# Performance work log

Measured on AMD Instinct MI355X. Metric: run time of the kernel, lower is better.

## Reference

```python
import jax, jax.numpy as jnp
import numpy as np

D_MODEL = 1024
N_HEADS = 16
D_HEAD = D_MODEL // N_HEADS


def setup_inputs() -> dict:
    key = jax.random.key(0)
    ks = jax.random.split(key, 11)
    B, S = 4, 2048
    scale = 1.0 / np.sqrt(D_MODEL)
    inp = {
        "query": jax.random.normal(ks[0], (B, S, D_MODEL), jnp.float32),
        "key": jax.random.normal(ks[1], (B, S, D_MODEL), jnp.float32),
        "value": jax.random.normal(ks[2], (B, S, D_MODEL), jnp.float32),
        "Wq": jax.random.normal(ks[3], (D_MODEL, D_MODEL), jnp.float32) * scale,
        "bq": jnp.zeros((D_MODEL,), jnp.float32),
        "Wk": jax.random.normal(ks[4], (D_MODEL, D_MODEL), jnp.float32) * scale,
        "bk": jnp.zeros((D_MODEL,), jnp.float32),
        "Wv": jax.random.normal(ks[5], (D_MODEL, D_MODEL), jnp.float32) * scale,
        "bv": jnp.zeros((D_MODEL,), jnp.float32),
        "Wo": jax.random.normal(ks[6], (D_MODEL, D_MODEL), jnp.float32) * scale,
        "bo": jnp.zeros((D_MODEL,), jnp.float32),
    }
    return inp


def _split_heads(x):
    b, s, _ = x.shape
    return x.reshape(b, s, N_HEADS, D_HEAD).transpose(0, 2, 1, 3)  # [b,h,s,dh]


def reference(query, key, value, Wq, bq, Wk, bk, Wv, bv, Wo, bo):
    Q = _split_heads(query @ Wq + bq)
    K = _split_heads(key @ Wk + bk)
    V = _split_heads(value @ Wv + bv)
    scores = jnp.einsum("bhqd,bhkd->bhqk", Q, K) / jnp.sqrt(jnp.float32(D_HEAD))
    attn = jax.nn.softmax(scores, axis=-1)  # dropout p=0 (eval)
    context = jnp.einsum("bhqk,bhkd->bhqd", attn, V)
    b, h, s, dh = context.shape
    context = context.transpose(0, 2, 1, 3).reshape(b, s, D_MODEL)
    return context @ Wo + bo
```

## Files before the change

### kernel.cpp

```cpp
#include <hip/hip_runtime.h>
#include <stdint.h>

#define DM 1024
#define SEQ 2048
#define MTOT 8192

typedef __attribute__((ext_vector_type(8))) short bf16x8;
typedef __attribute__((ext_vector_type(4))) float f32x4;
typedef __attribute__((ext_vector_type(16))) float f32x16;
typedef __attribute__((ext_vector_type(8))) unsigned short u16x8;
typedef __attribute__((ext_vector_type(4))) unsigned short u16x4;
typedef __attribute__((ext_vector_type(4))) uint32_t u32x4;

__device__ __forceinline__ unsigned short f2bf(float x) {
  uint32_t u = __builtin_bit_cast(uint32_t, x);
  u += 0x7fffu + ((u >> 16) & 1u);
  return (unsigned short)(u >> 16);
}

__device__ __forceinline__ uint32_t cvtpk_bf16(float lo, float hi) {
  uint32_t r;
  asm("v_cvt_pk_bf16_f32 %0, %1, %2" : "=v"(r) : "v"(lo), "v"(hi));
  return r;
}

__device__ __forceinline__ void gload16(void* lds, const void* g) {
  __builtin_amdgcn_global_load_lds(
      (const __attribute__((address_space(1))) void*)(uintptr_t)g,
      (__attribute__((address_space(3))) void*)(uintptr_t)lds,
      16, 0, 0);
}

__global__ __launch_bounds__(256)
void prep_w(const float* __restrict__ w0, const float* __restrict__ w1,
            const float* __restrict__ w2, const float* __restrict__ w3,
            unsigned short* __restrict__ Wt) {
  const int z = blockIdx.z;
  const float* W = z == 0 ? w0 : z == 1 ? w1 : z == 2 ? w2 : w3;
  unsigned short* out = Wt + (size_t)z * 1048576;
  __shared__ float tile[32][33];
  const int n0 = blockIdx.x * 32, k0 = blockIdx.y * 32;
  const int tx = threadIdx.x & 31, ty = threadIdx.x >> 5;
#pragma unroll
  for (int j = 0; j < 32; j += 8)
    tile[ty + j][tx] = W[(size_t)(k0 + ty + j) * DM + n0 + tx];
  __syncthreads();
#pragma unroll
  for (int j = 0; j < 32; j += 8)
    out[(size_t)(n0 + ty + j) * DM + k0 + tx] = f2bf(tile[tx][ty + j]);
}

__global__ __launch_bounds__(256)
void cvt_f32_bf16(const float* __restrict__ in, unsigned short* __restrict__ out, int n8) {
  int i = blockIdx.x * 256 + threadIdx.x;
  if (i < n8) {
    f32x4 a = *(const f32x4*)(in + (size_t)i * 8);
    f32x4 b = *(const f32x4*)(in + (size_t)i * 8 + 4);
    u16x8 o;
#pragma unroll
    for (int j = 0; j < 4; ++j) { o[j] = f2bf(a[j]); o[4 + j] = f2bf(b[j]); }
    *(u16x8*)(out + (size_t)i * 8) = o;
  }
}

template <int MODE>
__global__ __launch_bounds__(256)
void gemm_bt(const unsigned short* __restrict__ A,
             const unsigned short* __restrict__ Wt,
             const float* __restrict__ bias,
             void* __restrict__ C, float oscale) {
  __shared__ char sA[16384];
  __shared__ char sB[16384];
  const int t = threadIdx.x, wave = t >> 6, lane = t & 63;
  const int m0 = blockIdx.y * 128, n0 = blockIdx.x * 128;
  const int wr = (wave >> 1) * 64, wc = (wave & 1) * 64;
  const int lr = lane & 15, kg = lane >> 4;

  f32x4 acc[4][4];
#pragma unroll
  for (int i = 0; i < 4; ++i)
#pragma unroll
    for (int j = 0; j < 4; ++j) acc[i][j] = (f32x4){0.f, 0.f, 0.f, 0.f};

  for (int kt = 0; kt < 16; ++kt) {
    __syncthreads();
#pragma unroll
    for (int i = 0; i < 4; ++i) {
      int c = wave * 4 + i;
      int row = c * 8 + (lane >> 3);
      int bo = ((lane & 7) * 16) ^ ((row & 7) << 4);
      gload16(&sA[c * 1024], (const char*)(A + (size_t)(m0 + row) * DM + kt * 64) + bo);
      gload16(&sB[c * 1024], (const char*)(Wt + (size_t)(n0 + row) * DM + kt * 64) + bo);
    }
    __syncthreads();
#pragma unroll
    for (int ks = 0; ks < 2; ++ks) {
      bf16x8 afr[4], bfr[4];
#pragma unroll
      for (int j = 0; j < 4; ++j) {
        int mr = wr + j * 16 + lr;
        afr[j] = *(const bf16x8*)&sA[mr * 128 + ((ks * 64 + kg * 16) ^ ((mr & 7) << 4))];
        int nr = wc + j * 16 + lr;
        bfr[j] = *(const bf16x8*)&sB[nr * 128 + ((ks * 64 + kg * 16) ^ ((nr & 7) << 4))];
      }
#pragma unroll
      for (int mi = 0; mi < 4; ++mi)
#pragma unroll
        for (int nj = 0; nj < 4; ++nj)
          acc[mi][nj] = __builtin_amdgcn_mfma_f32_16x16x32_bf16(afr[mi], bfr[nj], acc[mi][nj], 0, 0, 0);
    }
  }
#pragma unroll
  for (int nj = 0; nj < 4; ++nj) {
    int col = n0 + wc + nj * 16 + lr;
    float bv = bias[col];
#pragma unroll
    for (int mi = 0; mi < 4; ++mi) {
      int rowseq = m0 + wr + mi * 16 + kg * 4;
      if (MODE == 2) {
        u16x4 pk;
#pragma unroll
        for (int r = 0; r < 4; ++r) pk[r] = f2bf(acc[mi][nj][r] + bv);
        *(u16x4*)((unsigned short*)C +
                  ((size_t)((rowseq >> 11) << 10) + col) * SEQ + (rowseq & 2047)) = pk;
      } else {
#pragma unroll
        for (int r = 0; r < 4; ++r) {
          float v = (acc[mi][nj][r] + bv) * oscale;
          if (MODE == 1) ((float*)C)[(size_t)(rowseq + r) * DM + col] = v;
          else ((unsigned short*)C)[(size_t)(rowseq + r) * DM + col] = f2bf(v);
        }
      }
    }
  }
}

__global__ __launch_bounds__(512)
void attn(const unsigned short* __restrict__ Qb,
          const unsigned short* __restrict__ Kb,
          const unsigned short* __restrict__ Vt,
          unsigned short* __restrict__ Ctx) {
  __shared__ char sK[2][8192];
  __shared__ char sV[2][8192];
  const int t = threadIdx.x, wave = t >> 6, lane = t & 63;
  const int l31 = lane & 31, hi = lane >> 5;
  const int bh = blockIdx.x, b = bh >> 4, h = bh & 15;
  const int q0 = blockIdx.y * 256;

  const int srow = wave * 8 + (lane >> 3);
  const int sbo = ((lane & 7) * 16) ^ ((srow & 7) << 4);
  const char* gK = (const char*)(Kb + (size_t)b * SEQ * DM + h * 64) + (size_t)srow * (DM * 2) + sbo;
  const char* gV = (const char*)(Vt + ((size_t)bh * 64 + srow) * SEQ) + sbo;

  bf16x8 qf[4];
  {
    const unsigned short* qp = Qb + ((size_t)b * SEQ + q0 + wave * 32 + l31) * DM + h * 64 + hi * 8;
#pragma unroll
    for (int ks = 0; ks < 4; ++ks) qf[ks] = *(const bf16x8*)(qp + ks * 16);
  }

  f32x16 ot0, ot1;
#pragma unroll
  for (int i = 0; i < 16; ++i) { ot0[i] = 0.f; ot1[i] = 0.f; }
  float m = -1e30f, l = 0.f;

  gload16(&sK[0][wave * 1024], gK);
  gload16(&sV[0][wave * 1024], gV);
  __syncthreads();

  for (int kt = 0; kt < SEQ / 64; ++kt) {
    const int pb = kt & 1;
    if (kt + 1 < SEQ / 64) {
      gload16(&sK[pb ^ 1][wave * 1024], gK + (size_t)(kt + 1) * 64 * (DM * 2));
      gload16(&sV[pb ^ 1][wave * 1024], gV + (size_t)(kt + 1) * 128);
    }

    f32x16 s0, s1;
#pragma unroll
    for (int i = 0; i < 16; ++i) { s0[i] = 0.f; s1[i] = 0.f; }
    const char* kbase = sK[pb];
#pragma unroll
    for (int ks = 0; ks < 4; ++ks) {
      const int swz = (ks * 32 + hi * 16) ^ ((l31 & 7) << 4);
      bf16x8 kf0 = *(const bf16x8*)(kbase + l31 * 128 + swz);
      s0 = __builtin_amdgcn_mfma_f32_32x32x16_bf16(kf0, qf[ks], s0, 0, 0, 0);
      bf16x8 kf1 = *(const bf16x8*)(kbase + (32 + l31) * 128 + swz);
      s1 = __builtin_amdgcn_mfma_f32_32x32x16_bf16(kf1, qf[ks], s1, 0, 0, 0);
    }

    float pmax = s0[0];
#pragma unroll
    for (int i = 1; i < 16; ++i) pmax = fmaxf(pmax, s0[i]);
#pragma unroll
    for (int i = 0; i < 16; ++i) pmax = fmaxf(pmax, s1[i]);
    pmax = fmaxf(pmax, __shfl_xor(pmax, 32));
    if (__any(pmax > m + 8.f)) {
      float mn = fmaxf(m, pmax);
      float al = __builtin_amdgcn_exp2f(m - mn);
      m = mn; l *= al;
#pragma unroll
      for (int i = 0; i < 16; ++i) { ot0[i] *= al; ot1[i] *= al; }
    }
    float sum = 0.f;
#pragma unroll
    for (int i = 0; i < 16; ++i) { float p = __builtin_amdgcn_exp2f(s0[i] - m); s0[i] = p; sum += p; }
#pragma unroll
    for (int i = 0; i < 16; ++i) { float p = __builtin_amdgcn_exp2f(s1[i] - m); s1[i] = p; sum += p; }
    sum += __shfl_xor(sum, 32);
    l += sum;

    const char* vbase = sV[pb];
#pragma unroll
    for (int sl = 0; sl < 4; ++sl) {
      const f32x16& sp = (sl < 2) ? s0 : s1;
      const int s8 = (sl & 1) * 8;
      uint32_t x0 = cvtpk_bf16(sp[s8 + 0], sp[s8 + 1]);
      uint32_t x1 = cvtpk_bf16(sp[s8 + 2], sp[s8 + 3]);
      uint32_t y0 = cvtpk_bf16(sp[s8 + 4], sp[s8 + 5]);
      uint32_t y1 = cvtpk_bf16(sp[s8 + 6], sp[s8 + 7]);
      uint32_t x0s = (uint32_t)__shfl_xor((int)x0, 32);
      uint32_t x1s = (uint32_t)__shfl_xor((int)x1, 32);
      uint32_t y0s = (uint32_t)__shfl_xor((int)y0, 32);
      uint32_t y1s = (uint32_t)__shfl_xor((int)y1, 32);
      u32x4 wv;
      wv[0] = hi ? y0s : x0;
      wv[1] = hi ? y1s : x1;
      wv[2] = hi ? y0 : x0s;
      wv[3] = hi ? y1 : x1s;
      bf16x8 pf = __builtin_bit_cast(bf16x8, wv);
      {
        const int swz = (sl * 32 + hi * 16) ^ ((l31 & 7) << 4);
        bf16x8 vf0 = *(const bf16x8*)(vbase + l31 * 128 + swz);
        ot0 = __builtin_amdgcn_mfma_f32_32x32x16_bf16(vf0, pf, ot0, 0, 0, 0);
        bf16x8 vf1 = *(const bf16x8*)(vbase + (32 + l31) * 128 + swz);
        ot1 = __builtin_amdgcn_mfma_f32_32x32x16_bf16(vf1, pf, ot1, 0, 0, 0);
      }
    }
    __syncthreads();
  }

  float inv = 1.0f / l;
  unsigned short* orow = Ctx + ((size_t)b * SEQ + q0 + wave * 32 + l31) * DM + h * 64;
#pragma unroll
  for (int dt = 0; dt < 2; ++dt) {
    const f32x16& o = dt ? ot1 : ot0;
#pragma unroll
    for (int rg = 0; rg < 4; ++rg) {
      u16x4 pk;
#pragma unroll
      for (int i = 0; i < 4; ++i) pk[i] = f2bf(o[rg * 4 + i] * inv);
      *(u16x4*)(orow + dt * 32 + rg * 8 + hi * 4) = pk;
    }
  }
}

extern "C" void kernel_launch(void* const* d_in, const int* in_sizes, int n_in,
                              void* d_out, int out_size, void* d_ws, size_t ws_size,
                              hipStream_t stream) {
  const float* query = (const float*)d_in[0];
  const float* key   = (const float*)d_in[1];
  const float* value = (const float*)d_in[2];
  const float* Wq = (const float*)d_in[3];
  const float* bq = (const float*)d_in[4];
  const float* Wk = (const float*)d_in[5];
  const float* bk = (const float*)d_in[6];
  const float* Wv = (const float*)d_in[7];
  const float* bv = (const float*)d_in[8];
  const float* Wo = (const float*)d_in[9];
  const float* bo = (const float*)d_in[10];

  char* ws = (char*)d_ws;
  unsigned short* Wt = (unsigned short*)ws;
  unsigned short* Qb = (unsigned short*)(ws + 8388608);
  unsigned short* Kb = (unsigned short*)(ws + 8388608 + 16777216);
  unsigned short* Vt = (unsigned short*)(ws + 8388608 + 2 * 16777216);
  unsigned short* Xc = (unsigned short*)(ws + 8388608 + 3 * 16777216);

  prep_w<<<dim3(32, 32, 4), 256, 0, stream>>>(Wq, Wk, Wv, Wo, Wt);

  const float QSCALE = 0.125f * 1.44269504088896340736f;
  cvt_f32_bf16<<<4096, 256, 0, stream>>>(query, Xc, MTOT * DM / 8);
  gemm_bt<0><<<dim3(8, 64), 256, 0, stream>>>(Xc, Wt, bq, Qb, QSCALE);
  cvt_f32_bf16<<<4096, 256, 0, stream>>>(key, Xc, MTOT * DM / 8);
  gemm_bt<0><<<dim3(8, 64), 256, 0, stream>>>(Xc, Wt + (size_t)1048576, bk, Kb, 1.0f);
  cvt_f32_bf16<<<4096, 256, 0, stream>>>(value, Xc, MTOT * DM / 8);
  gemm_bt<2><<<dim3(8, 64), 256, 0, stream>>>(Xc, Wt + (size_t)2 * 1048576, bv, Vt, 1.0f);

  attn<<<dim3(64, 8), 512, 0, stream>>>(Qb, Kb, Vt, Xc);

  gemm_bt<1><<<dim3(8, 64), 256, 0, stream>>>(Xc, Wt + (size_t)3 * 1048576, bo, d_out, 1.0f);
}
```

Baseline: 225.0 us.

## Shrink attention blocks to four waves, add setprio, reorder GEMM grid

The attention kernel drops to 256 threads covering 128 queries per block. Each wave now stages two K and two V rows per tile, and the grid doubles along the query axis. MFMA sections are wrapped in s_setprio, the row max uses a v_max3 tree, and the exp-sum uses four independent accumulators with the cross-half shuffle moved to the end of the loop. The GEMM grid is transposed so consecutive blocks walk M instead of N, which changes L2 reuse of the weight tiles. Together these aim for better occupancy, scheduling and ILP, at the cost of more blocks re-reading K/V.

```diff
diff --git a/kernel.cpp b/kernel.cpp
--- a/kernel.cpp
+++ b/kernel.cpp
@@ -21,6 +21,12 @@
 __device__ __forceinline__ uint32_t cvtpk_bf16(float lo, float hi) {
   uint32_t r;
   asm("v_cvt_pk_bf16_f32 %0, %1, %2" : "=v"(r) : "v"(lo), "v"(hi));
+  return r;
+}
+
+__device__ __forceinline__ float max3f(float a, float b, float c) {
+  float r;
+  asm("v_max3_f32 %0, %1, %2, %3" : "=v"(r) : "v"(a), "v"(b), "v"(c));
   return r;
 }
 
@@ -72,7 +78,7 @@
   __shared__ char sA[16384];
   __shared__ char sB[16384];
   const int t = threadIdx.x, wave = t >> 6, lane = t & 63;
-  const int m0 = blockIdx.y * 128, n0 = blockIdx.x * 128;
+  const int m0 = blockIdx.x * 128, n0 = blockIdx.y * 128;
   const int wr = (wave >> 1) * 64, wc = (wave & 1) * 64;
   const int lr = lane & 15, kg = lane >> 4;
 
@@ -135,7 +141,7 @@
   }
 }
 
-__global__ __launch_bounds__(512)
+__global__ __launch_bounds__(256)
 void attn(const unsigned short* __restrict__ Qb,
           const unsigned short* __restrict__ Kb,
           const unsigned short* __restrict__ Vt,
@@ -145,12 +151,19 @@
   const int t = threadIdx.x, wave = t >> 6, lane = t & 63;
   const int l31 = lane & 31, hi = lane >> 5;
   const int bh = blockIdx.x, b = bh >> 4, h = bh & 15;
-  const int q0 = blockIdx.y * 256;
-
-  const int srow = wave * 8 + (lane >> 3);
+  const int q0 = blockIdx.y * 128;
+
+  const int srow = wave * 16 + (lane >> 3);
   const int sbo = ((lane & 7) * 16) ^ ((srow & 7) << 4);
-  const char* gK = (const char*)(Kb + (size_t)b * SEQ * DM + h * 64) + (size_t)srow * (DM * 2) + sbo;
-  const char* gV = (const char*)(Vt + ((size_t)bh * 64 + srow) * SEQ) + sbo;
+  const char* gK = (const char*)Kb + ((size_t)b * SEQ + srow) * (DM * 2) + h * 128 + sbo;
+  const char* gV = (const char*)Vt + (((size_t)bh * 64 + srow)) * (SEQ * 2) + sbo;
+
+#define STAGE(buf, kt) do { \
+    gload16(&sK[buf][wave * 2048],        gK + (size_t)(kt) * 131072); \
+    gload16(&sK[buf][wave * 2048 + 1024], gK + (size_t)(kt) * 131072 + 16384); \
+    gload16(&sV[buf][wave * 2048],        gV + (size_t)(kt) * 128); \
+    gload16(&sV[buf][wave * 2048 + 1024], gV + (size_t)(kt) * 128 + 32768); \
+  } while (0)
 
   bf16x8 qf[4];
   {
@@ -164,21 +177,18 @@
   for (int i = 0; i < 16; ++i) { ot0[i] = 0.f; ot1[i] = 0.f; }
   float m = -1e30f, l = 0.f;
 
-  gload16(&sK[0][wave * 1024], gK);
-  gload16(&sV[0][wave * 1024], gV);
+  STAGE(0, 0);
   __syncthreads();
 
   for (int kt = 0; kt < SEQ / 64; ++kt) {
     const int pb = kt & 1;
-    if (kt + 1 < SEQ / 64) {
-      gload16(&sK[pb ^ 1][wave * 1024], gK + (size_t)(kt + 1) * 64 * (DM * 2));
-      gload16(&sV[pb ^ 1][wave * 1024], gV + (size_t)(kt + 1) * 128);
-    }
+    if (kt + 1 < SEQ / 64) STAGE(pb ^ 1, kt + 1);
 
     f32x16 s0, s1;
 #pragma unroll
     for (int i = 0; i < 16; ++i) { s0[i] = 0.f; s1[i] = 0.f; }
     const char* kbase = sK[pb];
+    __builtin_amdgcn_s_setprio(1);
 #pragma unroll
     for (int ks = 0; ks < 4; ++ks) {
       const int swz = (ks * 32 + hi * 16) ^ ((l31 & 7) << 4);
@@ -187,13 +197,16 @@
       bf16x8 kf1 = *(const bf16x8*)(kbase + (32 + l31) * 128 + swz);
       s1 = __builtin_amdgcn_mfma_f32_32x32x16_bf16(kf1, qf[ks], s1, 0, 0, 0);
     }
-
-    float pmax = s0[0];
-#pragma unroll
-    for (int i = 1; i < 16; ++i) pmax = fmaxf(pmax, s0[i]);
-#pragma unroll
-    for (int i = 0; i < 16; ++i) pmax = fmaxf(pmax, s1[i]);
+    __builtin_amdgcn_s_setprio(0);
+
+    float w[8];
+#pragma unroll
+    for (int i = 0; i < 8; ++i)
+      w[i] = fmaxf(fmaxf(s0[i], s0[i + 8]), fmaxf(s1[i], s1[i + 8]));
+    float pmax = fmaxf(max3f(w[0], w[1], w[2]), max3f(w[3], w[4], w[5]));
+    pmax = fmaxf(pmax, fmaxf(w[6], w[7]));
     pmax = fmaxf(pmax, __shfl_xor(pmax, 32));
+
     if (__any(pmax > m + 8.f)) {
       float mn = fmaxf(m, pmax);
       float al = __builtin_amdgcn_exp2f(m - mn);
@@ -201,13 +214,22 @@
 #pragma unroll
       for (int i = 0; i < 16; ++i) { ot0[i] *= al; ot1[i] *= al; }
     }
-    float sum = 0.f;
-#pragma unroll
-    for (int i = 0; i < 16; ++i) { float p = __builtin_amdgcn_exp2f(s0[i] - m); s0[i] = p; sum += p; }
-#pragma unroll
-    for (int i = 0; i < 16; ++i) { float p = __builtin_amdgcn_exp2f(s1[i] - m); s1[i] = p; sum += p; }
-    sum += __shfl_xor(sum, 32);
-    l += sum;
+    float su0 = 0.f, su1 = 0.f, su2 = 0.f, su3 = 0.f;
+#pragma unroll
+    for (int i = 0; i < 16; i += 4) {
+      float p0 = __builtin_amdgcn_exp2f(s0[i + 0] - m); s0[i + 0] = p0; su0 += p0;
+      float p1 = __builtin_amdgcn_exp2f(s0[i + 1] - m); s0[i + 1] = p1; su1 += p1;
+      float p2 = __builtin_amdgcn_exp2f(s0[i + 2] - m); s0[i + 2] = p2; su2 += p2;
+      float p3 = __builtin_amdgcn_exp2f(s0[i + 3] - m); s0[i + 3] = p3; su3 += p3;
+    }
+#pragma unroll
+    for (int i = 0; i < 16; i += 4) {
+      float p0 = __builtin_amdgcn_exp2f(s1[i + 0] - m); s1[i + 0] = p0; su0 += p0;
+      float p1 = __builtin_amdgcn_exp2f(s1[i + 1] - m); s1[i + 1] = p1; su1 += p1;
+      float p2 = __builtin_amdgcn_exp2f(s1[i + 2] - m); s1[i + 2] = p2; su2 += p2;
+      float p3 = __builtin_amdgcn_exp2f(s1[i + 3] - m); s1[i + 3] = p3; su3 += p3;
+    }
+    l += (su0 + su1) + (su2 + su3);
 
     const char* vbase = sV[pb];
 #pragma unroll
@@ -228,18 +250,20 @@
       wv[2] = hi ? y0 : x0s;
       wv[3] = hi ? y1 : x1s;
       bf16x8 pf = __builtin_bit_cast(bf16x8, wv);
-      {
-        const int swz = (sl * 32 + hi * 16) ^ ((l31 & 7) << 4);
-        bf16x8 vf0 = *(const bf16x8*)(vbase + l31 * 128 + swz);
-        ot0 = __builtin_amdgcn_mfma_f32_32x32x16_bf16(vf0, pf, ot0, 0, 0, 0);
-        bf16x8 vf1 = *(const bf16x8*)(vbase + (32 + l31) * 128 + swz);
-        ot1 = __builtin_amdgcn_mfma_f32_32x32x16_bf16(vf1, pf, ot1, 0, 0, 0);
-      }
+      const int swz = (sl * 32 + hi * 16) ^ ((l31 & 7) << 4);
+      bf16x8 vf0 = *(const bf16x8*)(vbase + l31 * 128 + swz);
+      bf16x8 vf1 = *(const bf16x8*)(vbase + (32 + l31) * 128 + swz);
+      __builtin_amdgcn_s_setprio(1);
+      ot0 = __builtin_amdgcn_mfma_f32_32x32x16_bf16(vf0, pf, ot0, 0, 0, 0);
+      ot1 = __builtin_amdgcn_mfma_f32_32x32x16_bf16(vf1, pf, ot1, 0, 0, 0);
+      __builtin_amdgcn_s_setprio(0);
     }
     __syncthreads();
   }
-
-  float inv = 1.0f / l;
+#undef STAGE
+
+  float lt = l + __shfl_xor(l, 32);
+  float inv = 1.0f / lt;
   unsigned short* orow = Ctx + ((size_t)b * SEQ + q0 + wave * 32 + l31) * DM + h * 64;
 #pragma unroll
   for (int dt = 0; dt < 2; ++dt) {
@@ -280,13 +304,13 @@
 
   const float QSCALE = 0.125f * 1.44269504088896340736f;
   cvt_f32_bf16<<<4096, 256, 0, stream>>>(query, Xc, MTOT * DM / 8);
-  gemm_bt<0><<<dim3(8, 64), 256, 0, stream>>>(Xc, Wt, bq, Qb, QSCALE);
+  gemm_bt<0><<<dim3(64, 8), 256, 0, stream>>>(Xc, Wt, bq, Qb, QSCALE);
   cvt_f32_bf16<<<4096, 256, 0, stream>>>(key, Xc, MTOT * DM / 8);
-  gemm_bt<0><<<dim3(8, 64), 256, 0, stream>>>(Xc, Wt + (size_t)1048576, bk, Kb, 1.0f);
+  gemm_bt<0><<<dim3(64, 8), 256, 0, stream>>>(Xc, Wt + (size_t)1048576, bk, Kb, 1.0f);
   cvt_f32_bf16<<<4096, 256, 0, stream>>>(value, Xc, MTOT * DM / 8);
-  gemm_bt<2><<<dim3(8, 64), 256, 0, stream>>>(Xc, Wt + (size_t)2 * 1048576, bv, Vt, 1.0f);
-
-  attn<<<dim3(64, 8), 512, 0, stream>>>(Qb, Kb, Vt, Xc);
-
-  gemm_bt<1><<<dim3(8, 64), 256, 0, stream>>>(Xc, Wt + (size_t)3 * 1048576, bo, d_out, 1.0f);
-}
+  gemm_bt<2><<<dim3(64, 8), 256, 0, stream>>>(Xc, Wt + (size_t)2 * 1048576, bv, Vt, 1.0f);
+
+  attn<<<dim3(64, 16), 256, 0, stream>>>(Qb, Kb, Vt, Xc);
+
+  gemm_bt<1><<<dim3(64, 8), 256, 0, stream>>>(Xc, Wt + (size_t)3 * 1048576, bo, d_out, 1.0f);
+}
```

After: 241.8 us. 1.07x slower.
